# Optimization experiments

Hardware: AMD Instinct MI355X
Metric: run time of the kernel (lower is better)

The kernel has to match this reference:

```python
import jax, jax.numpy as jnp
import numpy as np

DEL_ID, STOP_ID, PAD_ID, KEEP_ID = 3, 5, 0, 2


def lstm(x, h0, c0, Wi, Wh, bi, bh):
    """Single-layer batch-first LSTM, PyTorch gate order (i,f,g,o).
    x: [B,T,E]; h0,c0: [B,H]. Returns (ys [B,T,H], h [B,H], c [B,H])."""
    b = bi + bh

    def step(carry, xt):
        h, c = carry
        g = xt @ Wi.T + h @ Wh.T + b  # [B,4H]
        i, f, gg, o = jnp.split(g, 4, axis=-1)
        c = jax.nn.sigmoid(f) * c + jax.nn.sigmoid(i) * jnp.tanh(gg)
        h = jax.nn.sigmoid(o) * jnp.tanh(c)
        return (h, c), h

    (h, c), ys = jax.lax.scan(step, (h0, c0), jnp.swapaxes(x, 0, 1))
    return jnp.swapaxes(ys, 0, 1), h, c


def setup_inputs() -> dict:
    key = jax.random.key(0)
    ks = jax.random.split(key, 20)
    B, T, S, H, E, V = 32, 100, 100, 512, 256, 30000
    s = 0.02
    inp = {
        "input_edits": jax.random.randint(ks[0], (B, T), 0, V),
        "simp_sent": jax.random.randint(ks[1], (B, S), 0, V),
        "org_ids": jax.random.randint(ks[2], (B, S), 0, V),
        "encoder_outputs_org": jax.random.normal(ks[3], (B, S, H), dtype=jnp.float32),
        "h0": jnp.zeros((B, H), jnp.float32),
        "c0": jnp.zeros((B, H), jnp.float32),
        "emb": jax.random.normal(ks[4], (V, E), dtype=jnp.float32) * s,
        "Wi_e": jax.random.normal(ks[5], (4 * H, E), dtype=jnp.float32) * s,
        "Wh_e": jax.random.normal(ks[6], (4 * H, H), dtype=jnp.float32) * s,
        "bi_e": jnp.zeros((4 * H,), jnp.float32),
        "bh_e": jnp.zeros((4 * H,), jnp.float32),
        "Wi_w": jax.random.normal(ks[7], (4 * H, E), dtype=jnp.float32) * s,
        "Wh_w": jax.random.normal(ks[8], (4 * H, H), dtype=jnp.float32) * s,
        "bi_w": jnp.zeros((4 * H,), jnp.float32),
        "bh_w": jnp.zeros((4 * H,), jnp.float32),
        "Wp": jax.random.normal(ks[9], (H, H), dtype=jnp.float32) * s,
        "Wm": jax.random.normal(ks[10], (E, 4 * H), dtype=jnp.float32) * s,
        "bm": jnp.zeros((E,), jnp.float32),
        "b_out": jnp.zeros((30000,), jnp.float32),
    }
    return inp


def reference(input_edits, simp_sent, org_ids, encoder_outputs_org, h0, c0,
              emb, Wi_e, Wh_e, bi_e, bh_e, Wi_w, Wh_w, bi_w, bh_w,
              Wp, Wm, bm, b_out):
    # teacher_forcing_ratio = 1.0 -> teacher-forcing branch only
    B, T = input_edits.shape
    S = encoder_outputs_org.shape[1]
    Sw = simp_sent.shape[1]

    # run both LSTMs over the full teacher-forced sequences
    out_e, he, ce = lstm(emb[input_edits], h0, c0, Wi_e, Wh_e, bi_e, bh_e)  # [B,T,H]
    out_w, _, _ = lstm(emb[simp_sent], h0, c0, Wi_w, Wh_w, bi_w, bh_w)      # [B,Sw,H]

    # attention over encoder outputs
    key_org = out_e @ Wp.T                                                   # [B,T,H]
    attn = jax.nn.softmax(jnp.einsum('bth,bsh->bts', key_org, encoder_outputs_org), axis=-1)
    applied = jnp.einsum('bts,bsh->bth', attn, encoder_outputs_org)          # [B,T,H]

    # counters are exclusive cumsums of gold-action masks over input_edits[:,1:]
    a = input_edits[:, 1:]                                                   # gold actions, [B,T-1]
    inc_del = ((a == KEEP_ID) | (a == DEL_ID)).astype(jnp.int32)
    inc_ins = ((a != DEL_ID) & (a != STOP_ID) & (a != PAD_ID)).astype(jnp.int32)
    ctr_del = jnp.clip(jnp.cumsum(inc_del, 1) - inc_del, 0, S - 1)           # [B,T-1]
    ctr_ins = jnp.clip(jnp.cumsum(inc_ins, 1) - inc_ins, 0, Sw - 1)

    H = encoder_outputs_org.shape[2]
    c = jnp.take_along_axis(encoder_outputs_org,
                            jnp.broadcast_to(ctr_del[:, :, None], (B, T - 1, H)), axis=1)
    c_word = jnp.take_along_axis(out_w,
                                 jnp.broadcast_to(ctr_ins[:, :, None], (B, T - 1, H)), axis=1)

    feat = jnp.concatenate([out_e[:, :T - 1], applied[:, :T - 1], c, c_word], axis=-1)  # [B,T-1,4H]
    hmlp = jnp.tanh(feat @ Wm.T + bm)                                        # [B,T-1,E]
    logp = jax.nn.log_softmax(hmlp @ emb.T + b_out, axis=-1)                 # [B,T-1,V]
    return logp, he[None], ce[None]
```

## Files before the change

### kernel.cpp

```cpp
#include <hip/hip_runtime.h>
#include <math.h>


typedef __attribute__((ext_vector_type(8))) short short8v;
typedef __attribute__((ext_vector_type(4))) float f32x4;
typedef unsigned long long ull;

#define LSTM_BLOCKS 64
#define NTIL 235

__device__ __forceinline__ float sigf(float x){ return 1.0f/(1.0f + __expf(-x)); }
__device__ __forceinline__ float tanhc(float x){
  x = fminf(fmaxf(x, -15.f), 15.f);
  float e = __expf(2.f*x);
  return (e-1.f)/(e+1.f);
}
__device__ __forceinline__ short f2bf(float f){
  unsigned u = __float_as_uint(f);
  u = (u + 0x7fffu + ((u >> 16) & 1u)) >> 16;
  return (short)u;
}
__device__ __forceinline__ float bf2f(short s){
  return __uint_as_float(((unsigned)(unsigned short)s) << 16);
}

__global__ void prep_permute(const float* __restrict__ Wi, const float* __restrict__ Wh,
                             const float* __restrict__ bi, const float* __restrict__ bh,
                             short* __restrict__ WiPh, short* __restrict__ WhPh,
                             float* __restrict__ biasP)
{
  int idx = blockIdx.x*256 + threadIdx.x;
  {
    int op = idx >> 9, k = idx & 511;
    int u = op >> 2, g = op & 3;
    WhPh[idx] = f2bf(Wh[(g*512+u)*512 + k]);
  }
  if (idx < 2048*256) {
    int op = idx >> 8, e = idx & 255;
    int u = op >> 2, g = op & 3;
    WiPh[idx] = f2bf(Wi[(g*512+u)*256 + e]);
  }
  if (idx < 2048) {
    int u = idx >> 2, g = idx & 3;
    biasP[idx] = bi[g*512+u] + bh[g*512+u];
  }
}

__global__ void init_all(const float* __restrict__ h0, ull* __restrict__ hq,
                         unsigned* __restrict__ bar)
{
  int idx = blockIdx.x*256 + threadIdx.x;
  if (idx < 8192) {
    int b = (idx >> 7) & 31, q = idx & 127;
    const float* src = h0 + b*512 + q*4;
    ull v = ((ull)(unsigned short)f2bf(src[3]) << 48) |
            ((ull)(unsigned short)f2bf(src[2]) << 32) |
            ((ull)(unsigned short)f2bf(src[1]) << 16) |
            ((ull)(unsigned short)f2bf(src[0]));
    hq[idx] = v;
  }
  if (idx < 128) bar[idx] = 0u;
}

__global__ void conv_bf16(const float* __restrict__ src, short* __restrict__ dst, int n4)
{
  int i = blockIdx.x*256 + threadIdx.x;
  if (i >= n4) return;
  float4 v = *(const float4*)(src + (long)i*4);
  short4 o;
  o.x = f2bf(v.x); o.y = f2bf(v.y); o.z = f2bf(v.z); o.w = f2bf(v.w);
  *(short4*)(dst + (long)i*4) = o;
}

template<int GATHER,int CVT_A,int BIAS,int TANH,int OUT_BF16>
__global__ __launch_bounds__(256) void gemm_mfma(
    const void* __restrict__ Av, const int* __restrict__ tok,
    const short* __restrict__ Bh, const float* __restrict__ bias,
    void* __restrict__ Cv, int M, int N, int K, int lda, int ldc)
{
  __shared__ short As[128][72];
  __shared__ short Bs[128][72];
  const int bm = blockIdx.x * 128;
  const int bn = blockIdx.y * 128;
  const int tid = threadIdx.x;
  const int w = tid >> 6, l = tid & 63;
  const int wr = (w >> 1) * 64, wc = (w & 1) * 64;
  const int lr = l & 15, kg = l >> 4;

  f32x4 acc[4][4] = {};

  for (int k0 = 0; k0 < K; k0 += 64) {
    #pragma unroll
    for (int q = 0; q < 4; ++q) {
      int ci = tid + 256*q;
      int r = ci >> 3, ch = ci & 7;
      int ar = bm + r; if (ar > M-1) ar = M-1;
      if (GATHER) ar = tok[ar];
      if (CVT_A) {
        const float* ap = ((const float*)Av) + (long)ar*lda + k0 + ch*8;
        float4 v0 = *(const float4*)ap;
        float4 v1 = *(const float4*)(ap + 4);
        short8v s;
        s[0]=f2bf(v0.x); s[1]=f2bf(v0.y); s[2]=f2bf(v0.z); s[3]=f2bf(v0.w);
        s[4]=f2bf(v1.x); s[5]=f2bf(v1.y); s[6]=f2bf(v1.z); s[7]=f2bf(v1.w);
        *(short8v*)&As[r][ch*8] = s;
      } else {
        *(short8v*)&As[r][ch*8] =
            *(const short8v*)(((const short*)Av) + (long)ar*lda + k0 + ch*8);
      }
      int br = bn + r; if (br > N-1) br = N-1;
      *(short8v*)&Bs[r][ch*8] = *(const short8v*)(Bh + (long)br*K + k0 + ch*8);
    }
    __syncthreads();
    #pragma unroll
    for (int ks = 0; ks < 2; ++ks) {
      short8v a[4], b[4];
      #pragma unroll
      for (int m = 0; m < 4; ++m)
        a[m] = *(const short8v*)&As[wr + m*16 + lr][ks*32 + kg*8];
      #pragma unroll
      for (int n = 0; n < 4; ++n)
        b[n] = *(const short8v*)&Bs[wc + n*16 + lr][ks*32 + kg*8];
      #pragma unroll
      for (int m = 0; m < 4; ++m)
        #pragma unroll
        for (int n = 0; n < 4; ++n)
          acc[m][n] = __builtin_amdgcn_mfma_f32_16x16x32_bf16(a[m], b[n], acc[m][n], 0, 0, 0);
    }
    __syncthreads();
  }

  #pragma unroll
  for (int n = 0; n < 4; ++n) {
    int col = bn + wc + n*16 + lr;
    bool cok = (col < N);
    float bv = (BIAS && cok) ? bias[col] : 0.f;
    #pragma unroll
    for (int m = 0; m < 4; ++m) {
      int row0 = bm + wr + m*16 + kg*4;
      #pragma unroll
      for (int r = 0; r < 4; ++r) {
        int row = row0 + r;
        if (cok && row < M) {
          float v = acc[m][n][r] + bv;
          if (TANH) v = tanhc(v);
          if (OUT_BF16) ((short*)Cv)[(long)row*ldc + col] = f2bf(v);
          else          ((float*)Cv)[(long)row*ldc + col] = v;
        }
      }
    }
  }
}

__global__ __launch_bounds__(256) void logits_mfma_partial(
    const short* __restrict__ Ah,
    const short* __restrict__ Bh,
    const float* __restrict__ bias,
    short* __restrict__ Cg,
    float2* __restrict__ partial)
{
  __shared__ short As[128][72];
  __shared__ short Bs[128][72];
  __shared__ float2 red[128][2];
  const int bm = blockIdx.x * 128;
  const int bn = blockIdx.y * 128;
  const int tid = threadIdx.x;
  const int w = tid >> 6, l = tid & 63;
  const int wr = (w >> 1) * 64, wc = (w & 1) * 64;
  const int lr = l & 15, kg = l >> 4;

  f32x4 acc[4][4] = {};

  #pragma unroll
  for (int k0 = 0; k0 < 256; k0 += 64) {
    #pragma unroll
    for (int q = 0; q < 4; ++q) {
      int ci = tid + 256*q;
      int r = ci >> 3, ch = ci & 7;
      int ar = bm + r; if (ar > 3167) ar = 3167;
      *(short8v*)&As[r][ch*8] = *(const short8v*)(Ah + (long)ar*256 + k0 + ch*8);
      int br = bn + r; if (br > 29999) br = 29999;
      *(short8v*)&Bs[r][ch*8] = *(const short8v*)(Bh + (long)br*256 + k0 + ch*8);
    }
    __syncthreads();
    #pragma unroll
    for (int ks = 0; ks < 2; ++ks) {
      short8v a[4], b[4];
      #pragma unroll
      for (int m = 0; m < 4; ++m)
        a[m] = *(const short8v*)&As[wr + m*16 + lr][ks*32 + kg*8];
      #pragma unroll
      for (int n = 0; n < 4; ++n)
        b[n] = *(const short8v*)&Bs[wc + n*16 + lr][ks*32 + kg*8];
      #pragma unroll
      for (int m = 0; m < 4; ++m)
        #pragma unroll
        for (int n = 0; n < 4; ++n)
          acc[m][n] = __builtin_amdgcn_mfma_f32_16x16x32_bf16(a[m], b[n], acc[m][n], 0, 0, 0);
    }
    __syncthreads();
  }

  #pragma unroll
  for (int n = 0; n < 4; ++n) {
    int col = bn + wc + n*16 + lr;
    float bv = (col < 30000) ? bias[col] : 0.f;
    #pragma unroll
    for (int m = 0; m < 4; ++m)
      #pragma unroll
      for (int r = 0; r < 4; ++r)
        acc[m][n][r] = (col < 30000) ? acc[m][n][r] + bv : -INFINITY;
  }
  #pragma unroll
  for (int m = 0; m < 4; ++m) {
    #pragma unroll
    for (int r = 0; r < 4; ++r) {
      float a0 = acc[m][0][r], a1 = acc[m][1][r], a2 = acc[m][2][r], a3 = acc[m][3][r];
      float mx = fmaxf(fmaxf(a0, a1), fmaxf(a2, a3));
      #pragma unroll
      for (int off = 1; off < 16; off <<= 1) mx = fmaxf(mx, __shfl_xor(mx, off));
      float se = 0.f;
      if (mx > -INFINITY)
        se = __expf(a0-mx) + __expf(a1-mx) + __expf(a2-mx) + __expf(a3-mx);
      #pragma unroll
      for (int off = 1; off < 16; off <<= 1) se += __shfl_xor(se, off);
      if (lr == 0) red[wr + m*16 + kg*4 + r][w & 1] = make_float2(mx, se);
    }
  }
  #pragma unroll
  for (int n = 0; n < 4; ++n) {
    int col = bn + wc + n*16 + lr;
    if (col < 30000) {
      #pragma unroll
      for (int m = 0; m < 4; ++m) {
        int row0 = bm + wr + m*16 + kg*4;
        #pragma unroll
        for (int r = 0; r < 4; ++r) {
          int row = row0 + r;
          if (row < 3168) Cg[(long)row*30000 + col] = f2bf(acc[m][n][r]);
        }
      }
    }
  }
  __syncthreads();
  if (tid < 128) {
    int row = bm + tid;
    if (row < 3168) {
      float2 A = red[tid][0], B = red[tid][1];
      float M = fmaxf(A.x, B.x);
      float S = 0.f;
      if (M > -INFINITY) S = A.y*__expf(A.x - M) + B.y*__expf(B.x - M);
      partial[(long)row*NTIL + blockIdx.y] = make_float2(M, S);
    }
  }
}

__global__ void lse_reduce(const float2* __restrict__ partial, float* __restrict__ lse)
{
  int row  = blockIdx.x*4 + (threadIdx.x >> 6);
  int lane = threadIdx.x & 63;
  if (row >= 3168) return;
  const float2* pr = partial + (long)row*NTIL;
  float m = -INFINITY, s = 0.f;
  for (int tl = lane; tl < NTIL; tl += 64) {
    float2 p = pr[tl];
    float nm = fmaxf(m, p.x);
    if (nm > -INFINITY) {
      s = s*__expf(m - nm) + p.y*__expf(p.x - nm);
      m = nm;
    }
  }
  #pragma unroll
  for (int off = 32; off; off >>= 1) {
    float om = __shfl_xor(m, off);
    float os = __shfl_xor(s, off);
    float nm = fmaxf(m, om);
    if (nm > -INFINITY) {
      s = s*__expf(m - nm) + os*__expf(om - nm);
      m = nm;
    }
  }
  if (lane == 0) lse[row] = m + __logf(s);
}

__global__ __launch_bounds__(256) void sub_lse_bf16(const short* __restrict__ Cg,
                                                    const float* __restrict__ lse,
                                                    float* __restrict__ out)
{
  int row = blockIdx.x;
  float lv = lse[row];
  const short* src = Cg + (long)row*30000;
  float* dst = out + (long)row*30000;
  for (int i = threadIdx.x; i < 3750; i += 256) {
    short8v v = *(const short8v*)(src + i*8);
    float4 o0, o1;
    o0.x = bf2f(v[0]) - lv; o0.y = bf2f(v[1]) - lv;
    o0.z = bf2f(v[2]) - lv; o0.w = bf2f(v[3]) - lv;
    o1.x = bf2f(v[4]) - lv; o1.y = bf2f(v[5]) - lv;
    o1.z = bf2f(v[6]) - lv; o1.w = bf2f(v[7]) - lv;
    *(float4*)(dst + i*8)     = o0;
    *(float4*)(dst + i*8 + 4) = o1;
  }
}

template<int TRANSB>
__global__ __launch_bounds__(256) void gemm_f32(
    const float* __restrict__ A, const float* __restrict__ Bmat,
    float* __restrict__ C,
    int M, int N, int K, int lda, int ldb, int ldc,
    long sA, long sB, long sC)
{
  __shared__ float As[32][68];
  __shared__ float Bs[32][68];
  const int z = blockIdx.z;
  A    += (long)z * sA;
  Bmat += (long)z * sB;
  C    += (long)z * sC;
  const int bm = blockIdx.y*64, bn = blockIdx.x*64;
  const int tid = threadIdx.x;
  const int tx = tid & 15, ty = tid >> 4;
  float acc[4][4] = {};

  for (int k0 = 0; k0 < K; k0 += 32) {
    {
      int r = tid >> 2;
      int c0 = (tid & 3) * 8;
      int row = bm + r; if (row > M-1) row = M-1;
      const float* ap = A + (long)row * lda;
      #pragma unroll
      for (int q = 0; q < 2; ++q) {
        int kk = c0 + q*4;
        float4 v;
        if (k0 + kk + 4 <= K) v = *(const float4*)(ap + k0 + kk);
        else {
          v.x = (k0+kk+0 < K) ? ap[k0+kk+0] : 0.f;
          v.y = (k0+kk+1 < K) ? ap[k0+kk+1] : 0.f;
          v.z = (k0+kk+2 < K) ? ap[k0+kk+2] : 0.f;
          v.w = (k0+kk+3 < K) ? ap[k0+kk+3] : 0.f;
        }
        As[kk+0][r]=v.x; As[kk+1][r]=v.y; As[kk+2][r]=v.z; As[kk+3][r]=v.w;
      }
    }
    if (TRANSB) {
      int n = tid >> 2;
      int c0 = (tid & 3) * 8;
      int col = bn + n; if (col > N-1) col = N-1;
      const float* bp = Bmat + (long)col * ldb;
      #pragma unroll
      for (int q = 0; q < 2; ++q) {
        int kk = c0 + q*4;
        float4 v;
        if (k0 + kk + 4 <= K) v = *(const float4*)(bp + k0 + kk);
        else {
          v.x = (k0+kk+0 < K) ? bp[k0+kk+0] : 0.f;
          v.y = (k0+kk+1 < K) ? bp[k0+kk+1] : 0.f;
          v.z = (k0+kk+2 < K) ? bp[k0+kk+2] : 0.f;
          v.w = (k0+kk+3 < K) ? bp[k0+kk+3] : 0.f;
        }
        Bs[kk+0][n]=v.x; Bs[kk+1][n]=v.y; Bs[kk+2][n]=v.z; Bs[kk+3][n]=v.w;
      }
    } else {
      int kk = tid >> 3;
      int c0 = (tid & 7) * 8;
      int krow = k0 + kk;
      #pragma unroll
      for (int q = 0; q < 2; ++q) {
        int cc = c0 + q*4;
        int col = bn + cc;
        float4 v = make_float4(0.f,0.f,0.f,0.f);
        if (krow < K) {
          const float* bp = Bmat + (long)krow * ldb;
          if (col + 4 <= N) v = *(const float4*)(bp + col);
          else {
            v.x = (col+0 < N) ? bp[col+0] : 0.f;
            v.y = (col+1 < N) ? bp[col+1] : 0.f;
            v.z = (col+2 < N) ? bp[col+2] : 0.f;
            v.w = (col+3 < N) ? bp[col+3] : 0.f;
          }
        }
        Bs[kk][cc+0]=v.x; Bs[kk][cc+1]=v.y; Bs[kk][cc+2]=v.z; Bs[kk][cc+3]=v.w;
      }
    }
    __syncthreads();
    #pragma unroll
    for (int kk = 0; kk < 32; ++kk) {
      float4 a = *(const float4*)&As[kk][ty*4];
      float4 b = *(const float4*)&Bs[kk][tx*4];
      acc[0][0]=fmaf(a.x,b.x,acc[0][0]); acc[0][1]=fmaf(a.x,b.y,acc[0][1]);
      acc[0][2]=fmaf(a.x,b.z,acc[0][2]); acc[0][3]=fmaf(a.x,b.w,acc[0][3]);
      acc[1][0]=fmaf(a.y,b.x,acc[1][0]); acc[1][1]=fmaf(a.y,b.y,acc[1][1]);
      acc[1][2]=fmaf(a.y,b.z,acc[1][2]); acc[1][3]=fmaf(a.y,b.w,acc[1][3]);
      acc[2][0]=fmaf(a.z,b.x,acc[2][0]); acc[2][1]=fmaf(a.z,b.y,acc[2][1]);
      acc[2][2]=fmaf(a.z,b.z,acc[2][2]); acc[2][3]=fmaf(a.z,b.w,acc[2][3]);
      acc[3][0]=fmaf(a.w,b.x,acc[3][0]); acc[3][1]=fmaf(a.w,b.y,acc[3][1]);
      acc[3][2]=fmaf(a.w,b.z,acc[3][2]); acc[3][3]=fmaf(a.w,b.w,acc[3][3]);
    }
    __syncthreads();
  }
  #pragma unroll
  for (int i = 0; i < 4; ++i) {
    int row = bm + ty*4 + i;
    if (row >= M) continue;
    #pragma unroll
    for (int j = 0; j < 4; ++j) {
      int col = bn + tx*4 + j;
      if (col >= N) continue;
      C[(long)row*ldc + col] = acc[i][j];
    }
  }
}

__global__ __launch_bounds__(256, 1) void lstm_persist(
    const short* __restrict__ WhPh_e, const short* __restrict__ WhPh_w,
    const float* __restrict__ Xp_e, const float* __restrict__ Xp_w,
    const float* __restrict__ c0_in,
    ull* __restrict__ hq,
    short* __restrict__ outT,
    float* __restrict__ out_hc,
    unsigned* __restrict__ flags)
{
  const int bx = blockIdx.x;
  const int l = bx >> 5;
  const int ublk = bx & 31;
  const int tid = threadIdx.x;
  const int w = tid >> 6, lane = tid & 63;
  const int uloc = lane >> 4;
  const int bn = lane & 15;
  const int u_global = ublk*16 + w*4 + uloc;
  const int ob = (ublk*16 + w*4) * 4;
  const int qcol = ublk*4 + w;

  const short* WhPh = l ? WhPh_w : WhPh_e;
  const float* Xp   = l ? Xp_w   : Xp_e;
  const unsigned* myfl = flags + l*32;

  __shared__ short hT[32][520];

  __hip_atomic_load(&flags[100], __ATOMIC_ACQUIRE, __HIP_MEMORY_SCOPE_AGENT);

  short8v afr[16];
  {
    const short* wp = WhPh + (long)(ob + bn)*512 + (lane >> 4)*8;
    #pragma unroll
    for (int ks = 0; ks < 16; ++ks)
      afr[ks] = *(const short8v*)(wp + ks*32);
  }
  float c_s0 = c0_in[bn*512 + u_global];
  float c_s1 = c0_in[(bn+16)*512 + u_global];

  for (int t = 0; t < 100; ++t) {
    float4 x0 = *(const float4*)(Xp + ((long)(bn*100 + t))*2048 + u_global*4);
    float4 x1 = *(const float4*)(Xp + ((long)((bn+16)*100 + t))*2048 + u_global*4);
    if (t) {
      int ok;
      do {
        unsigned f = (lane < 32)
          ? __hip_atomic_load(&myfl[lane], __ATOMIC_RELAXED, __HIP_MEMORY_SCOPE_AGENT)
          : 0xffffffffu;
        ok = __all((int)(f >= (unsigned)t));
        if (!ok) __builtin_amdgcn_s_sleep(1);
      } while (!ok);
    }
    {
      const ull* hsrc = hq + (size_t)t*8192 + (l << 12);
      #pragma unroll
      for (int i = 0; i < 16; ++i) {
        int idx = tid + 256*i;
        int b = idx >> 7, q = idx & 127;
        *(ull*)&hT[b][q*4] = hsrc[idx];
      }
    }
    __syncthreads();
    f32x4 acc0 = {}, acc1 = {};
    #pragma unroll
    for (int ks = 0; ks < 16; ++ks) {
      short8v b0 = *(const short8v*)&hT[bn][ks*32 + (lane>>4)*8];
      short8v b1 = *(const short8v*)&hT[bn+16][ks*32 + (lane>>4)*8];
      acc0 = __builtin_amdgcn_mfma_f32_16x16x32_bf16(afr[ks], b0, acc0, 0, 0, 0);
      acc1 = __builtin_amdgcn_mfma_f32_16x16x32_bf16(afr[ks], b1, acc1, 0, 0, 0);
    }
    float gi = acc0[0] + x0.x, gf = acc0[1] + x0.y, gg = acc0[2] + x0.z, go = acc0[3] + x0.w;
    c_s0 = sigf(gf)*c_s0 + sigf(gi)*tanhc(gg);
    float hv0 = sigf(go)*tanhc(c_s0);
    gi = acc1[0] + x1.x; gf = acc1[1] + x1.y; gg = acc1[2] + x1.z; go = acc1[3] + x1.w;
    c_s1 = sigf(gf)*c_s1 + sigf(gi)*tanhc(gg);
    float hv1 = sigf(go)*tanhc(c_s1);

    short hb0 = f2bf(hv0), hb1 = f2bf(hv1);
    unsigned p0 = (unsigned)(unsigned short)hb0;
    unsigned p1 = (unsigned)(unsigned short)hb1;
    unsigned a1 = __shfl_down((int)p0, 16), a2 = __shfl_down((int)p0, 32), a3 = __shfl_down((int)p0, 48);
    unsigned e1 = __shfl_down((int)p1, 16), e2 = __shfl_down((int)p1, 32), e3 = __shfl_down((int)p1, 48);
    if (uloc == 0) {
      ull q0 = ((ull)((a2 & 0xffffu) | (a3 << 16)) << 32) | ((p0 & 0xffffu) | (a1 << 16));
      ull q1 = ((ull)((e2 & 0xffffu) | (e3 << 16)) << 32) | ((p1 & 0xffffu) | (e1 << 16));
      ull* hd = hq + (size_t)(t+1)*8192 + (l << 12);
      __hip_atomic_store(&hd[(bn << 7) + qcol],      q0, __ATOMIC_RELAXED, __HIP_MEMORY_SCOPE_AGENT);
      __hip_atomic_store(&hd[((bn+16) << 7) + qcol], q1, __ATOMIC_RELAXED, __HIP_MEMORY_SCOPE_AGENT);
    }
    short* od = outT + ((long)(l*100 + t)*512 + u_global)*32;
    od[bn]    = hb0;
    od[bn+16] = hb1;
    if (t == 99 && l == 0) {
      out_hc[bn*512 + u_global]              = hv0;
      out_hc[(bn+16)*512 + u_global]         = hv1;
      out_hc[16384 + bn*512 + u_global]      = c_s0;
      out_hc[16384 + (bn+16)*512 + u_global] = c_s1;
    }
    if (t < 99) {
      asm volatile("s_waitcnt vmcnt(0)" ::: "memory");
      __syncthreads();
      if (tid == 0)
        __hip_atomic_store(&flags[bx], (unsigned)(t+1),
                           __ATOMIC_RELAXED, __HIP_MEMORY_SCOPE_AGENT);
    }
  }
}

__global__ __launch_bounds__(256) void transpose_out(
    const short* __restrict__ outT, short* __restrict__ out_e, short* __restrict__ out_w)
{
  __shared__ short tile[512][40];
  const int t = blockIdx.x, l = blockIdx.y;
  const short* src = outT + (long)(l*100 + t)*16384;
  const int tid = threadIdx.x;
  #pragma unroll
  for (int i = 0; i < 8; ++i) {
    int fi = tid + 256*i;
    int u = fi >> 2, b8 = (fi & 3)*8;
    *(short8v*)&tile[u][b8] = *(const short8v*)(src + fi*8);
  }
  __syncthreads();
  short* dst = l ? out_w : out_e;
  for (int b = 0; b < 32; ++b) {
    short* drow = dst + (long)(b*100 + t)*512;
    drow[tid]     = tile[tid][b];
    drow[tid+256] = tile[tid+256][b];
  }
}

__global__ void softmax_rows(float* __restrict__ P)
{
  int row  = blockIdx.x*4 + (threadIdx.x >> 6);
  int lane = threadIdx.x & 63;
  float* p = P + (long)row*128;
  float x0 = (lane      < 100) ? p[lane]    : -INFINITY;
  float x1 = (lane + 64 < 100) ? p[lane+64] : -INFINITY;
  float m = fmaxf(x0, x1);
  #pragma unroll
  for (int off = 32; off; off >>= 1) m = fmaxf(m, __shfl_xor(m, off));
  float e0 = (lane      < 100) ? __expf(x0 - m) : 0.f;
  float e1 = (lane + 64 < 100) ? __expf(x1 - m) : 0.f;
  float s = e0 + e1;
  #pragma unroll
  for (int off = 32; off; off >>= 1) s += __shfl_xor(s, off);
  float inv = 1.f / s;
  if (lane      < 100) p[lane]    = e0 * inv;
  if (lane + 64 < 100) p[lane+64] = e1 * inv;
}

__global__ void counters_kernel(const int* __restrict__ ie,
                                int* __restrict__ ctr_del, int* __restrict__ ctr_ins)
{
  int b = threadIdx.x;
  if (b >= 32) return;
  int rd = 0, ri = 0;
  for (int t = 0; t < 99; ++t) {
    int a = ie[b*100 + t + 1];
    int incd = (a == 2 || a == 3) ? 1 : 0;
    int inci = (a != 3 && a != 5 && a != 0) ? 1 : 0;
    ctr_del[b*99 + t] = min(rd, 99);
    ctr_ins[b*99 + t] = min(ri, 99);
    rd += incd; ri += inci;
  }
}

__global__ void feat_kernel(const short* __restrict__ out_e, const float* __restrict__ applied,
                            const float* __restrict__ enc,  const short* __restrict__ out_w,
                            const int* __restrict__ ctr_del, const int* __restrict__ ctr_ins,
                            short* __restrict__ feat)
{
  int n = blockIdx.x;
  int b = n / 99, t = n % 99;
  int tid = threadIdx.x;
  int seg = tid >> 6;
  int off = (tid & 63) * 8;
  short8v v;
  if (seg == 0) {
    v = *(const short8v*)(out_e + (long)(b*100 + t)*512 + off);
  } else if (seg == 3) {
    v = *(const short8v*)(out_w + (long)(b*100 + ctr_ins[n])*512 + off);
  } else {
    const float* s = (seg == 1) ? applied + (long)(b*100 + t)*512
                                : enc     + (long)(b*100 + ctr_del[n])*512;
    float4 v0 = *(const float4*)(s + off);
    float4 v1 = *(const float4*)(s + off + 4);
    v[0]=f2bf(v0.x); v[1]=f2bf(v0.y); v[2]=f2bf(v0.z); v[3]=f2bf(v0.w);
    v[4]=f2bf(v1.x); v[5]=f2bf(v1.y); v[6]=f2bf(v1.z); v[7]=f2bf(v1.w);
  }
  *(short8v*)(feat + (long)n*2048 + seg*512 + off) = v;
}

extern "C" void kernel_launch(void* const* d_in, const int* in_sizes, int n_in,
                              void* d_out, int out_size, void* d_ws, size_t ws_size,
                              hipStream_t stream)
{
  const int*   input_edits = (const int*)  d_in[0];
  const int*   simp_sent   = (const int*)  d_in[1];
  const float* enc   = (const float*)d_in[3];
  const float* h0    = (const float*)d_in[4];
  const float* c0    = (const float*)d_in[5];
  const float* emb   = (const float*)d_in[6];
  const float* Wi_e  = (const float*)d_in[7];
  const float* Wh_e  = (const float*)d_in[8];
  const float* bi_e  = (const float*)d_in[9];
  const float* bh_e  = (const float*)d_in[10];
  const float* Wi_w  = (const float*)d_in[11];
  const float* Wh_w  = (const float*)d_in[12];
  const float* bi_w  = (const float*)d_in[13];
  const float* bh_w  = (const float*)d_in[14];
  const float* Wp    = (const float*)d_in[15];
  const float* Wm    = (const float*)d_in[16];
  const float* bmv   = (const float*)d_in[17];
  const float* b_out = (const float*)d_in[18];
  float* out = (float*)d_out;

  float* ws = (float*)d_ws;
  size_t off = 0;
  auto alloc = [&](size_t n){ float* p = ws + off; off += (n + 63) & ~(size_t)63; return p; };

  short* WiPh_e   = (short*)alloc(262144);
  short* WiPh_w   = (short*)alloc(262144);
  float* biasP_e  = alloc(2048);
  float* biasP_w  = alloc(2048);
  short* WhPh_e   = (short*)alloc(524288);
  short* WhPh_w   = (short*)alloc(524288);
  float* Xp_e     = alloc(3200*2048);
  float* Xp_w     = alloc(3200*2048);
  short* outT     = (short*)alloc(1638400);
  short* out_e    = (short*)alloc(819200);
  short* out_w    = (short*)alloc(819200);
  ull*   hq       = (ull*)alloc(101*8192*2);
  unsigned* bar   = (unsigned*)alloc(128);
  float* Pbuf     = alloc(3200*128);
  float* lse      = alloc(3168);
  int*   ctr_del  = (int*)alloc(3168);
  int*   ctr_ins  = (int*)alloc(3168);
  short* Wph      = (short*)alloc(131072);
  short* Wmh      = (short*)alloc(262144);
  float* key      = alloc(3200*512);
  float* applied  = alloc(3200*512);
  short* logith   = (short*)alloc(47520000);
  float2* partial = (float2*)alloc(3168*NTIL*2);
  short* feath    = (short*)Xp_e;
  short* hmlph    = (short*)Xp_w;
  short* embh     = (short*)(Xp_w + 1048576);

  prep_permute<<<4096, 256, 0, stream>>>(Wi_e, Wh_e, bi_e, bh_e, WiPh_e, WhPh_e, biasP_e);
  prep_permute<<<4096, 256, 0, stream>>>(Wi_w, Wh_w, bi_w, bh_w, WiPh_w, WhPh_w, biasP_w);
  init_all<<<32, 256, 0, stream>>>(h0, hq, bar);
  conv_bf16<<<256, 256, 0, stream>>>(Wp, Wph, 512*512/4);
  conv_bf16<<<512, 256, 0, stream>>>(Wm, Wmh, 256*2048/4);

  gemm_mfma<1,1,1,0,0><<<dim3(25,16), 256, 0, stream>>>(
      emb, input_edits, WiPh_e, biasP_e, Xp_e, 3200, 2048, 256, 256, 2048);
  gemm_mfma<1,1,1,0,0><<<dim3(25,16), 256, 0, stream>>>(
      emb, simp_sent,   WiPh_w, biasP_w, Xp_w, 3200, 2048, 256, 256, 2048);

  lstm_persist<<<LSTM_BLOCKS, 256, 0, stream>>>(
      WhPh_e, WhPh_w, Xp_e, Xp_w, c0, hq, outT, out + 95040000L, bar);

  conv_bf16<<<7500, 256, 0, stream>>>(emb, embh, 30000*256/4);

  transpose_out<<<dim3(100,2), 256, 0, stream>>>(outT, out_e, out_w);

  gemm_mfma<0,0,0,0,0><<<dim3(25,4), 256, 0, stream>>>(
      out_e, nullptr, Wph, nullptr, key, 3200, 512, 512, 512, 512);

  gemm_f32<1><<<dim3(2,2,32), 256, 0, stream>>>(
      key, enc, Pbuf, 100, 100, 512, 512, 512, 128, 51200, 51200, 12800);
  softmax_rows<<<800, 256, 0, stream>>>(Pbuf);
  gemm_f32<0><<<dim3(8,2,32), 256, 0, stream>>>(
      Pbuf, enc, applied, 100, 512, 100, 128, 512, 512, 12800, 51200, 51200);

  counters_kernel<<<1, 64, 0, stream>>>(input_edits, ctr_del, ctr_ins);
  feat_kernel<<<3168, 256, 0, stream>>>(out_e, applied, enc, out_w, ctr_del, ctr_ins, feath);
  gemm_mfma<0,0,1,1,1><<<dim3(25,2), 256, 0, stream>>>(
      feath, nullptr, Wmh, bmv, hmlph, 3168, 256, 2048, 2048, 256);

  logits_mfma_partial<<<dim3(25, NTIL), 256, 0, stream>>>(
      hmlph, embh, b_out, logith, partial);
  lse_reduce<<<792, 256, 0, stream>>>(partial, lse);
  sub_lse_bf16<<<3168, 256, 0, stream>>>(logith, lse, out);
}
```

Baseline: 964.4 us.

## Merge prep launches and read LSTM hidden state directly from global memory

Several small prep kernels (weight permutes, bf16 conversions, h0 init, barrier reset, counters) are merged into two launches, and the two input-projection GEMMs become a single launch using a z grid dimension. This cuts kernel launch count and serial gaps. In the persistent LSTM, the per-step staging of h through LDS and its __syncthreads are removed: each lane loads its MFMA B fragments straight from the global hq buffer. The step-completion flag is now published before the outT and final-state stores, so dependent blocks can start sooner. The trade-off is more redundant global/L2 reads of h per block.

Result: slower. 1.262 ms (+30.9%).

```diff
diff --git a/kernel.cpp b/kernel.cpp
--- a/kernel.cpp
+++ b/kernel.cpp
@@ -24,11 +24,23 @@
   return __uint_as_float(((unsigned)(unsigned short)s) << 16);
 }
 
-__global__ void prep_permute(const float* __restrict__ Wi, const float* __restrict__ Wh,
-                             const float* __restrict__ bi, const float* __restrict__ bh,
-                             short* __restrict__ WiPh, short* __restrict__ WhPh,
-                             float* __restrict__ biasP)
-{
+__global__ void prep_permute(
+    const float* __restrict__ Wi_e, const float* __restrict__ Wh_e,
+    const float* __restrict__ bi_e, const float* __restrict__ bh_e,
+    const float* __restrict__ Wi_w, const float* __restrict__ Wh_w,
+    const float* __restrict__ bi_w, const float* __restrict__ bh_w,
+    short* __restrict__ WiPh_e, short* __restrict__ WhPh_e, float* __restrict__ biasP_e,
+    short* __restrict__ WiPh_w, short* __restrict__ WhPh_w, float* __restrict__ biasP_w)
+{
+  const int z = blockIdx.y;
+  const float* Wi = z ? Wi_w : Wi_e;
+  const float* Wh = z ? Wh_w : Wh_e;
+  const float* bi = z ? bi_w : bi_e;
+  const float* bh = z ? bh_w : bh_e;
+  short* WiPh = z ? WiPh_w : WiPh_e;
+  short* WhPh = z ? WhPh_w : WhPh_e;
+  float* biasP = z ? biasP_w : biasP_e;
+
   int idx = blockIdx.x*256 + threadIdx.x;
   {
     int op = idx >> 9, k = idx & 511;
@@ -46,20 +58,45 @@
   }
 }
 
-__global__ void init_all(const float* __restrict__ h0, ull* __restrict__ hq,
-                         unsigned* __restrict__ bar)
+__global__ void misc_prep(const float* __restrict__ Wp, const float* __restrict__ Wm,
+                          const float* __restrict__ h0, const int* __restrict__ ie,
+                          short* __restrict__ Wph, short* __restrict__ Wmh,
+                          ull* __restrict__ hq, unsigned* __restrict__ bar,
+                          int* __restrict__ ctr_del, int* __restrict__ ctr_ins)
 {
   int idx = blockIdx.x*256 + threadIdx.x;
-  if (idx < 8192) {
-    int b = (idx >> 7) & 31, q = idx & 127;
+  if (idx < 65536) {
+    float4 v = *(const float4*)(Wp + (long)idx*4);
+    short4 o; o.x=f2bf(v.x); o.y=f2bf(v.y); o.z=f2bf(v.z); o.w=f2bf(v.w);
+    *(short4*)(Wph + (long)idx*4) = o;
+  } else if (idx < 196608) {
+    int i = idx - 65536;
+    float4 v = *(const float4*)(Wm + (long)i*4);
+    short4 o; o.x=f2bf(v.x); o.y=f2bf(v.y); o.z=f2bf(v.z); o.w=f2bf(v.w);
+    *(short4*)(Wmh + (long)i*4) = o;
+  } else if (idx < 204800) {
+    int i = idx - 196608;
+    int b = (i >> 7) & 31, q = i & 127;
     const float* src = h0 + b*512 + q*4;
     ull v = ((ull)(unsigned short)f2bf(src[3]) << 48) |
             ((ull)(unsigned short)f2bf(src[2]) << 32) |
             ((ull)(unsigned short)f2bf(src[1]) << 16) |
             ((ull)(unsigned short)f2bf(src[0]));
-    hq[idx] = v;
-  }
-  if (idx < 128) bar[idx] = 0u;
+    hq[i] = v;
+  } else if (idx < 204928) {
+    bar[idx - 204800] = 0u;
+  } else if (idx < 204960) {
+    int b = idx - 204928;
+    int rd = 0, ri = 0;
+    for (int t = 0; t < 99; ++t) {
+      int a = ie[b*100 + t + 1];
+      int incd = (a == 2 || a == 3) ? 1 : 0;
+      int inci = (a != 3 && a != 5 && a != 0) ? 1 : 0;
+      ctr_del[b*99 + t] = min(rd, 99);
+      ctr_ins[b*99 + t] = min(ri, 99);
+      rd += incd; ri += inci;
+    }
+  }
 }
 
 __global__ void conv_bf16(const float* __restrict__ src, short* __restrict__ dst, int n4)
@@ -73,15 +110,16 @@
 }
 
 template<int GATHER,int CVT_A,int BIAS,int TANH,int OUT_BF16>
-__global__ __launch_bounds__(256) void gemm_mfma(
+__device__ __forceinline__ void gemm_mfma_body(
     const void* __restrict__ Av, const int* __restrict__ tok,
     const short* __restrict__ Bh, const float* __restrict__ bias,
-    void* __restrict__ Cv, int M, int N, int K, int lda, int ldc)
+    void* __restrict__ Cv, int M, int N, int K, int lda, int ldc,
+    int bxk, int byk)
 {
   __shared__ short As[128][72];
   __shared__ short Bs[128][72];
-  const int bm = blockIdx.x * 128;
-  const int bn = blockIdx.y * 128;
+  const int bm = bxk * 128;
+  const int bn = byk * 128;
   const int tid = threadIdx.x;
   const int w = tid >> 6, l = tid & 63;
   const int wr = (w >> 1) * 64, wc = (w & 1) * 64;
@@ -152,6 +190,30 @@
   }
 }
 
+template<int GATHER,int CVT_A,int BIAS,int TANH,int OUT_BF16>
+__global__ __launch_bounds__(256) void gemm_mfma(
+    const void* __restrict__ Av, const int* __restrict__ tok,
+    const short* __restrict__ Bh, const float* __restrict__ bias,
+    void* __restrict__ Cv, int M, int N, int K, int lda, int ldc)
+{
+  gemm_mfma_body<GATHER,CVT_A,BIAS,TANH,OUT_BF16>(
+      Av, tok, Bh, bias, Cv, M, N, K, lda, ldc, blockIdx.x, blockIdx.y);
+}
+
+__global__ __launch_bounds__(256) void xproj_mfma(
+    const float* __restrict__ emb,
+    const int* __restrict__ tokA, const int* __restrict__ tokB,
+    const short* __restrict__ WA, const short* __restrict__ WB,
+    const float* __restrict__ bA, const float* __restrict__ bB,
+    float* __restrict__ outA, float* __restrict__ outB)
+{
+  const int z = blockIdx.z;
+  gemm_mfma_body<1,1,1,0,0>(
+      emb, z ? tokB : tokA, z ? WB : WA, z ? bB : bA,
+      z ? (void*)outB : (void*)outA, 3200, 2048, 256, 256, 2048,
+      blockIdx.x, blockIdx.y);
+}
+
 __global__ __launch_bounds__(256) void logits_mfma_partial(
     const short* __restrict__ Ah,
     const short* __restrict__ Bh,
@@ -434,13 +496,11 @@
   const float* Xp   = l ? Xp_w   : Xp_e;
   const unsigned* myfl = flags + l*32;
 
-  __shared__ short hT[32][520];
-
   __hip_atomic_load(&flags[100], __ATOMIC_ACQUIRE, __HIP_MEMORY_SCOPE_AGENT);
 
   short8v afr[16];
   {
-    const short* wp = WhPh + (long)(ob + bn)*512 + (lane >> 4)*8;
+    const short* wp = WhPh + (long)(ob + bn)*512 + uloc*8;
     #pragma unroll
     for (int ks = 0; ks < 16; ++ks)
       afr[ks] = *(const short8v*)(wp + ks*32);
@@ -461,21 +521,14 @@
         if (!ok) __builtin_amdgcn_s_sleep(1);
       } while (!ok);
     }
-    {
-      const ull* hsrc = hq + (size_t)t*8192 + (l << 12);
-      #pragma unroll
-      for (int i = 0; i < 16; ++i) {
-        int idx = tid + 256*i;
-        int b = idx >> 7, q = idx & 127;
-        *(ull*)&hT[b][q*4] = hsrc[idx];
-      }
-    }
-    __syncthreads();
+    const ull* hsrc = hq + (size_t)t*8192 + (l << 12);
+    const ull* r0 = hsrc + (bn << 7) + uloc*2;
+    const ull* r1 = hsrc + ((bn+16) << 7) + uloc*2;
     f32x4 acc0 = {}, acc1 = {};
     #pragma unroll
     for (int ks = 0; ks < 16; ++ks) {
-      short8v b0 = *(const short8v*)&hT[bn][ks*32 + (lane>>4)*8];
-      short8v b1 = *(const short8v*)&hT[bn+16][ks*32 + (lane>>4)*8];
+      short8v b0 = *(const short8v*)(r0 + ks*8);
+      short8v b1 = *(const short8v*)(r1 + ks*8);
       acc0 = __builtin_amdgcn_mfma_f32_16x16x32_bf16(afr[ks], b0, acc0, 0, 0, 0);
       acc1 = __builtin_amdgcn_mfma_f32_16x16x32_bf16(afr[ks], b1, acc1, 0, 0, 0);
     }
@@ -498,6 +551,13 @@
       __hip_atomic_store(&hd[(bn << 7) + qcol],      q0, __ATOMIC_RELAXED, __HIP_MEMORY_SCOPE_AGENT);
       __hip_atomic_store(&hd[((bn+16) << 7) + qcol], q1, __ATOMIC_RELAXED, __HIP_MEMORY_SCOPE_AGENT);
     }
+    if (t < 99) {
+      asm volatile("s_waitcnt vmcnt(0)" ::: "memory");
+      __syncthreads();
+      if (tid == 0)
+        __hip_atomic_store(&flags[bx], (unsigned)(t+1),
+                           __ATOMIC_RELAXED, __HIP_MEMORY_SCOPE_AGENT);
+    }
     short* od = outT + ((long)(l*100 + t)*512 + u_global)*32;
     od[bn]    = hb0;
     od[bn+16] = hb1;
@@ -507,13 +567,6 @@
       out_hc[16384 + bn*512 + u_global]      = c_s0;
       out_hc[16384 + (bn+16)*512 + u_global] = c_s1;
     }
-    if (t < 99) {
-      asm volatile("s_waitcnt vmcnt(0)" ::: "memory");
-      __syncthreads();
-      if (tid == 0)
-        __hip_atomic_store(&flags[bx], (unsigned)(t+1),
-                           __ATOMIC_RELAXED, __HIP_MEMORY_SCOPE_AGENT);
-    }
   }
 }
 
@@ -557,22 +610,6 @@
   float inv = 1.f / s;
   if (lane      < 100) p[lane]    = e0 * inv;
   if (lane + 64 < 100) p[lane+64] = e1 * inv;
-}
-
-__global__ void counters_kernel(const int* __restrict__ ie,
-                                int* __restrict__ ctr_del, int* __restrict__ ctr_ins)
-{
-  int b = threadIdx.x;
-  if (b >= 32) return;
-  int rd = 0, ri = 0;
-  for (int t = 0; t < 99; ++t) {
-    int a = ie[b*100 + t + 1];
-    int incd = (a == 2 || a == 3) ? 1 : 0;
-    int inci = (a != 3 && a != 5 && a != 0) ? 1 : 0;
-    ctr_del[b*99 + t] = min(rd, 99);
-    ctr_ins[b*99 + t] = min(ri, 99);
-    rd += incd; ri += inci;
-  }
 }
 
 __global__ void feat_kernel(const short* __restrict__ out_e, const float* __restrict__ applied,
@@ -656,16 +693,14 @@
   short* hmlph    = (short*)Xp_w;
   short* embh     = (short*)(Xp_w + 1048576);
 
-  prep_permute<<<4096, 256, 0, stream>>>(Wi_e, Wh_e, bi_e, bh_e, WiPh_e, WhPh_e, biasP_e);
-  prep_permute<<<4096, 256, 0, stream>>>(Wi_w, Wh_w, bi_w, bh_w, WiPh_w, WhPh_w, biasP_w);
-  init_all<<<32, 256, 0, stream>>>(h0, hq, bar);
-  conv_bf16<<<256, 256, 0, stream>>>(Wp, Wph, 512*512/4);
-  conv_bf16<<<512, 256, 0, stream>>>(Wm, Wmh, 256*2048/4);
-
-  gemm_mfma<1,1,1,0,0><<<dim3(25,16), 256, 0, stream>>>(
-      emb, input_edits, WiPh_e, biasP_e, Xp_e, 3200, 2048, 256, 256, 2048);
-  gemm_mfma<1,1,1,0,0><<<dim3(25,16), 256, 0, stream>>>(
-      emb, simp_sent,   WiPh_w, biasP_w, Xp_w, 3200, 2048, 256, 256, 2048);
+  prep_permute<<<dim3(4096,2), 256, 0, stream>>>(
+      Wi_e, Wh_e, bi_e, bh_e, Wi_w, Wh_w, bi_w, bh_w,
+      WiPh_e, WhPh_e, biasP_e, WiPh_w, WhPh_w, biasP_w);
+  misc_prep<<<801, 256, 0, stream>>>(Wp, Wm, h0, input_edits,
+                                     Wph, Wmh, hq, bar, ctr_del, ctr_ins);
+
+  xproj_mfma<<<dim3(25,16,2), 256, 0, stream>>>(
+      emb, input_edits, simp_sent, WiPh_e, WiPh_w, biasP_e, biasP_w, Xp_e, Xp_w);
 
   lstm_persist<<<LSTM_BLOCKS, 256, 0, stream>>>(
       WhPh_e, WhPh_w, Xp_e, Xp_w, c0, hq, outT, out + 95040000L, bar);
@@ -683,7 +718,6 @@
   gemm_f32<0><<<dim3(8,2,32), 256, 0, stream>>>(
       Pbuf, enc, applied, 100, 512, 100, 128, 512, 512, 12800, 51200, 51200);
 
-  counters_kernel<<<1, 64, 0, stream>>>(input_edits, ctr_del, ctr_ins);
   feat_kernel<<<3168, 256, 0, stream>>>(out_e, applied, enc, out_w, ctr_del, ctr_ins, feath);
   gemm_mfma<0,0,1,1,1><<<dim3(25,2), 256, 0, stream>>>(
       feath, nullptr, Wmh, bmv, hmlph, 3168, 256, 2048, 2048, 256);
```
